# Kernel optimization log

Hardware: AMD Instinct MI355X
Metric: run time of the kernel (lower is better)

## Reference

```python
import jax, jax.numpy as jnp
import numpy as np

D_MODEL = 128
NUM_HEADS = 8
HEAD_DIM = D_MODEL // NUM_HEADS
LN_EPS = 1e-5


def layernorm(x, gamma, beta):
    mu = jnp.mean(x, axis=-1, keepdims=True)
    var = jnp.mean(jnp.square(x - mu), axis=-1, keepdims=True)
    return (x - mu) * jax.lax.rsqrt(var + LN_EPS) * gamma + beta


def setup_inputs() -> dict:
    key = jax.random.key(0)
    ks = jax.random.split(key, 12)
    B, L, d = 16, 1024, D_MODEL
    scale = 1.0 / np.sqrt(d)
    edge_x = jax.random.normal(ks[0], (B, L, d), dtype=jnp.float32)
    # True entries are masked out (masked_fill with -inf)
    edge_mask = jax.random.randint(ks[1], (B, L, L), 0, 2).astype(jnp.bool_)
    in_proj_w = jax.random.normal(ks[2], (d, 3 * d), dtype=jnp.float32) * scale  # fused QKV
    in_proj_b = jnp.zeros((3 * d,), dtype=jnp.float32)
    w1 = jax.random.normal(ks[3], (d, d), dtype=jnp.float32) * scale
    b1 = jnp.zeros((d,), dtype=jnp.float32)
    w2 = jax.random.normal(ks[4], (d, d), dtype=jnp.float32) * scale
    b2 = jnp.zeros((d,), dtype=jnp.float32)
    g1 = jnp.ones((d,), dtype=jnp.float32)
    beta1 = jnp.zeros((d,), dtype=jnp.float32)
    g2 = jnp.ones((d,), dtype=jnp.float32)
    beta2 = jnp.zeros((d,), dtype=jnp.float32)
    return {"edge_x": edge_x, "edge_mask": edge_mask, "in_proj_w": in_proj_w,
            "in_proj_b": in_proj_b, "w1": w1, "b1": b1, "w2": w2, "b2": b2,
            "g1": g1, "beta1": beta1, "g2": g2, "beta2": beta2}


def reference(edge_x, edge_mask, in_proj_w, in_proj_b, w1, b1, w2, b2, g1, beta1, g2, beta2):
    B, L, d = edge_x.shape
    H, hd = NUM_HEADS, HEAD_DIM
    scaling = float(hd) ** -0.5
    # fused QKV projection
    qkv = edge_x @ in_proj_w + in_proj_b              # [B, L, 3d]
    q, k, v = jnp.split(qkv, 3, axis=-1)
    q = q.reshape(B, L, H, hd).transpose(0, 2, 1, 3)  # [B, H, L, hd]
    k = k.reshape(B, L, H, hd).transpose(0, 2, 1, 3)
    v = v.reshape(B, L, H, hd).transpose(0, 2, 1, 3)
    scores = jnp.einsum('bhqd,bhkd->bhqk', q, k) * scaling  # [B, H, L, L]
    scores = jnp.where(edge_mask[:, None, :, :], -jnp.inf, scores)
    attn = jax.nn.softmax(scores, axis=-1)
    ctx = jnp.einsum('bhqk,bhkd->bhqd', attn, v)      # [B, H, L, hd]
    ctx = ctx.transpose(0, 2, 1, 3).reshape(B, L, d)
    # residual + LayerNorm
    x = layernorm(edge_x + ctx, g1, beta1)
    # FFN (relu), residual + LayerNorm (dropout=0 in eval mode)
    ff = jax.nn.relu(x @ w1 + b1) @ w2 + b2
    x = layernorm(x + ff, g2, beta2)
    return x
```

## Files before the change

### kernel.cpp

```cpp
#include <hip/hip_runtime.h>
#include <cstdint>

#define NROWS 16384
#define ARRE ((size_t)NROWS * 128)

typedef short short8 __attribute__((ext_vector_type(8)));
typedef float f32x4  __attribute__((ext_vector_type(4)));
typedef float f32x16 __attribute__((ext_vector_type(16)));

static __device__ __forceinline__ unsigned short f2bf(float f) {
    union { float f; uint32_t u; } v; v.f = f;
    uint32_t r = v.u + 0x7fffu + ((v.u >> 16) & 1u);
    return (unsigned short)(r >> 16);
}

__global__ void k_detect(const uint32_t* __restrict__ m, int* __restrict__ flag) {
    if (threadIdx.x == 0) {
        int f = 0;
        for (int i = 0; i < 256; ++i) f |= (m[i] > 1u) ? 1 : 0;
        *flag = f;
    }
}

__global__ void k_castw(const float* __restrict__ wqkv, const float* __restrict__ w1,
                        const float* __restrict__ w2, unsigned short* __restrict__ wT)
{
    const int e = blockIdx.x * 256 + threadIdx.x;
    if (e < 49152) {
        const int n = e >> 7, k = e & 127;
        wT[e] = f2bf(wqkv[k * 384 + n]);
    } else if (e < 65536) {
        const int i = e - 49152, n = i >> 7, k = i & 127;
        wT[e] = f2bf(w1[k * 128 + n]);
    } else if (e < 81920) {
        const int i = e - 65536, n = i >> 7, k = i & 127;
        wT[e] = f2bf(w2[k * 128 + n]);
    }
}

template<int NF, int MODE>
__global__ __launch_bounds__(256, 2) void k_mm(const float* __restrict__ Xf,
        const unsigned short* __restrict__ Wt, const float* __restrict__ bias,
        unsigned short* __restrict__ out)
{
    __shared__ char smem[16384 + NF * 4096];
    char* const sX = smem;
    char* const sW = smem + 16384;
    const int t = threadIdx.x;
    const int w = t >> 6, l = t & 63;
    const int l4 = l >> 4, l15 = l & 15;
    const int r0 = blockIdx.x * 64;
    const int c0 = blockIdx.y * (NF * 16);

    #pragma unroll
    for (int i = 0; i < 4; ++i) {
        const int c = t + 256 * i;
        const int row = c >> 4, slot = c & 15;
        const float4* src = (const float4*)(Xf + (size_t)(r0 + row) * 128 + slot * 8);
        float4 f0 = src[0], f1 = src[1];
        uint4 v;
        v.x = (uint32_t)f2bf(f0.x) | ((uint32_t)f2bf(f0.y) << 16);
        v.y = (uint32_t)f2bf(f0.z) | ((uint32_t)f2bf(f0.w) << 16);
        v.z = (uint32_t)f2bf(f1.x) | ((uint32_t)f2bf(f1.y) << 16);
        v.w = (uint32_t)f2bf(f1.z) | ((uint32_t)f2bf(f1.w) << 16);
        *(uint4*)(sX + row * 256 + ((slot ^ (row & 15)) << 4)) = v;
    }
    #pragma unroll
    for (int i = 0; i < NF; ++i) {
        const int c = t + 256 * i;
        const int col = c >> 4, slot = c & 15;
        uint4 v = *(const uint4*)(Wt + (size_t)(c0 + col) * 128 + slot * 8);
        *(uint4*)(sW + col * 256 + ((slot ^ (col & 15)) << 4)) = v;
    }
    __syncthreads();

    short8 aF[4];
    #pragma unroll
    for (int kk = 0; kk < 4; ++kk)
        aF[kk] = *(const short8*)(sX + (w * 16 + l15) * 256 + (((kk * 4 + l4) ^ l15) << 4));

    f32x4 acc[NF];
    #pragma unroll
    for (int nf = 0; nf < NF; ++nf) acc[nf] = f32x4{0.f, 0.f, 0.f, 0.f};
    #pragma unroll
    for (int nf = 0; nf < NF; ++nf) {
        #pragma unroll
        for (int kk = 0; kk < 4; ++kk) {
            short8 bF = *(const short8*)(sW + (nf * 16 + l15) * 256 + (((kk * 4 + l4) ^ l15) << 4));
            acc[nf] = __builtin_amdgcn_mfma_f32_16x16x32_bf16(aF[kk], bF, acc[nf], 0, 0, 0);
        }
    }

    const float scl = (MODE == 0 && blockIdx.y == 0) ? 0.25f : 1.0f;
    #pragma unroll
    for (int nf = 0; nf < NF; ++nf) {
        const int col = c0 + nf * 16 + l15;
        const float bv = bias[col];
        #pragma unroll
        for (int reg = 0; reg < 4; ++reg) {
            float v = acc[nf][reg] + bv;
            if (MODE == 1) v = fmaxf(v, 0.f);
            v *= scl;
            const int row = r0 + w * 16 + l4 * 4 + reg;
            size_t o;
            if (MODE == 0) o = (size_t)(col >> 7) * ARRE + (size_t)row * 128 + (col & 127);
            else           o = (size_t)row * 128 + col;
            out[o] = f2bf(v);
        }
    }
}

__global__ __launch_bounds__(256, 2) void k_mm2(const unsigned short* __restrict__ h1,
        const unsigned short* __restrict__ w2t, const float* __restrict__ b2,
        const float* __restrict__ x1, const float* __restrict__ g2,
        const float* __restrict__ be2, float* __restrict__ out)
{
    __shared__ char smem[16384 + 32768];
    char* const sX = smem;
    char* const sW = smem + 16384;
    const int t = threadIdx.x;
    const int w = t >> 6, l = t & 63;
    const int l4 = l >> 4, l15 = l & 15;
    const int r0 = blockIdx.x * 64;

    #pragma unroll
    for (int i = 0; i < 4; ++i) {
        const int c = t + 256 * i;
        const int row = c >> 4, slot = c & 15;
        uint4 v = *(const uint4*)(h1 + (size_t)(r0 + row) * 128 + slot * 8);
        *(uint4*)(sX + row * 256 + ((slot ^ (row & 15)) << 4)) = v;
    }
    #pragma unroll
    for (int i = 0; i < 8; ++i) {
        const int c = t + 256 * i;
        const int col = c >> 4, slot = c & 15;
        uint4 v = *(const uint4*)(w2t + (size_t)col * 128 + slot * 8);
        *(uint4*)(sW + col * 256 + ((slot ^ (col & 15)) << 4)) = v;
    }
    __syncthreads();

    short8 aF[4];
    #pragma unroll
    for (int kk = 0; kk < 4; ++kk)
        aF[kk] = *(const short8*)(sX + (w * 16 + l15) * 256 + (((kk * 4 + l4) ^ l15) << 4));

    f32x4 acc[8];
    #pragma unroll
    for (int nf = 0; nf < 8; ++nf) acc[nf] = f32x4{0.f, 0.f, 0.f, 0.f};
    #pragma unroll
    for (int nf = 0; nf < 8; ++nf) {
        #pragma unroll
        for (int kk = 0; kk < 4; ++kk) {
            short8 bF = *(const short8*)(sW + (nf * 16 + l15) * 256 + (((kk * 4 + l4) ^ l15) << 4));
            acc[nf] = __builtin_amdgcn_mfma_f32_16x16x32_bf16(aF[kk], bF, acc[nf], 0, 0, 0);
        }
    }

    float b2c[8], g2c[8], bec[8];
    #pragma unroll
    for (int nf = 0; nf < 8; ++nf) {
        const int col = nf * 16 + l15;
        b2c[nf] = b2[col]; g2c[nf] = g2[col]; bec[nf] = be2[col];
    }
    float y[8][4];
    #pragma unroll
    for (int nf = 0; nf < 8; ++nf) {
        const int col = nf * 16 + l15;
        #pragma unroll
        for (int reg = 0; reg < 4; ++reg) {
            const int row = r0 + w * 16 + l4 * 4 + reg;
            y[nf][reg] = acc[nf][reg] + b2c[nf] + x1[(size_t)row * 128 + col];
        }
    }
    #pragma unroll
    for (int reg = 0; reg < 4; ++reg) {
        float s = 0.f;
        #pragma unroll
        for (int nf = 0; nf < 8; ++nf) s += y[nf][reg];
        s += __shfl_xor(s, 1); s += __shfl_xor(s, 2);
        s += __shfl_xor(s, 4); s += __shfl_xor(s, 8);
        const float mu = s * (1.f / 128.f);
        float vv = 0.f;
        #pragma unroll
        for (int nf = 0; nf < 8; ++nf) { float d = y[nf][reg] - mu; vv += d * d; }
        vv += __shfl_xor(vv, 1); vv += __shfl_xor(vv, 2);
        vv += __shfl_xor(vv, 4); vv += __shfl_xor(vv, 8);
        const float rs = rsqrtf(vv * (1.f / 128.f) + 1e-5f);
        const int row = r0 + w * 16 + l4 * 4 + reg;
        #pragma unroll
        for (int nf = 0; nf < 8; ++nf) {
            const int col = nf * 16 + l15;
            out[(size_t)row * 128 + col] = (y[nf][reg] - mu) * rs * g2c[nf] + bec[nf];
        }
    }
}

__global__ __launch_bounds__(256, 2) void k_attn(
        const unsigned short* __restrict__ qb,
        const unsigned short* __restrict__ kb,
        const unsigned short* __restrict__ vbp,
        const void* __restrict__ maskp, const int* __restrict__ flag,
        const float* __restrict__ x, const float* __restrict__ g1,
        const float* __restrict__ be1, float* __restrict__ x1)
{
    __shared__ alignas(16) char smem[39072];
    char*          const sK = smem;
    char*          const sV = smem + 8192;
    char*          const sP = smem + 17440;
    unsigned char* const sM = (unsigned char*)(smem + 37920);
    float*         const sS = (float*)(smem + 38048);

    const int t  = threadIdx.x;
    const int w  = t >> 6;
    const int l  = t & 63;
    const int b  = blockIdx.y;
    const int q0 = blockIdx.x * 32;
    const int q   = l & 31;
    const int hi  = l >> 5;
    const int l4  = l >> 4;
    const int l15 = l & 15;
    const int bytemask = *flag;

    short8 qf0, qf1;
    {
        const size_t qrow = (size_t)(b * 1024 + q0 + q) * 128;
        qf0 = *(const short8*)(qb + qrow + (2 * w + 0) * 16 + hi * 8);
        qf1 = *(const short8*)(qb + qrow + (2 * w + 1) * 16 + hi * 8);
    }
    float m0 = -INFINITY, m1 = -INFINITY;
    float ls0 = 0.f, ls1 = 0.f;
    f32x4 a00 = {0,0,0,0}, a01 = {0,0,0,0}, a10 = {0,0,0,0}, a11 = {0,0,0,0};
    const f32x16 z16 = {};
    float* const sS0 = sS + (w * 2 + 0) * 32;
    float* const sS1 = sS + (w * 2 + 1) * 32;
    char*  const sP0 = sP + (w * 2 + 0) * 2560;
    char*  const sP1 = sP + (w * 2 + 1) * 2560;

    const uint8_t* m8  = (const uint8_t*)maskp;
    const int*     m32 = (const int*)maskp;

    uint32_t mks = 0;

    auto head_step = [&](int h, short8 qf, float& m, float& ls,
                         f32x4& ac0, f32x4& ac1, float* sSw, char* Pw) {
        short8 kf = *(const short8*)(sK + q * 256 + ((((h << 1) + hi) ^ (q & 15)) << 4));
        f32x16 sc = __builtin_amdgcn_mfma_f32_32x32x16_bf16(kf, qf, z16, 0, 0, 0);
        float sm = sc[0];
        #pragma unroll
        for (int r = 1; r < 16; ++r) sm = fmaxf(sm, sc[r]);
        sm = fmaxf(sm, __shfl_xor(sm, 32));
        if (__any(sm > m + 8.f)) {
            float nm = fmaxf(m, sm);
            float s  = __expf(m - nm);
            m = nm; ls *= s;
            sSw[q] = s;
            float4 s0v = *(float4*)&sSw[l4 * 4];
            float4 s1v = *(float4*)&sSw[l4 * 4 + 16];
            ac0[0] *= s0v.x; ac0[1] *= s0v.y; ac0[2] *= s0v.z; ac0[3] *= s0v.w;
            ac1[0] *= s1v.x; ac1[1] *= s1v.y; ac1[2] *= s1v.z; ac1[3] *= s1v.w;
        }
        float p[16]; float lsum = 0.f;
        #pragma unroll
        for (int r = 0; r < 16; ++r) {
            const int c = (r & 3) + 8 * (r >> 2);
            float pv = __expf(sc[r] - m);
            pv = ((mks >> c) & 1u) ? pv : 0.f;
            lsum += pv; p[r] = pv;
        }
        ls += lsum;
        #pragma unroll
        for (int g = 0; g < 4; ++g) {
            uint2 pk;
            pk.x = (uint32_t)f2bf(p[4*g+0]) | ((uint32_t)f2bf(p[4*g+1]) << 16);
            pk.y = (uint32_t)f2bf(p[4*g+2]) | ((uint32_t)f2bf(p[4*g+3]) << 16);
            *(uint2*)(Pw + q * 80 + (8 * g + 4 * hi) * 2) = pk;
        }
        short8 pa0 = *(const short8*)(Pw + l15 * 80 + l4 * 16);
        short8 pa1 = *(const short8*)(Pw + (l15 + 16) * 80 + l4 * 16);
        const unsigned short* sVh = (const unsigned short*)(sV + h * 1156);
        short8 vf;
        #pragma unroll
        for (int j = 0; j < 8; ++j)
            vf[j] = (short)sVh[(l4 * 8 + j) * 18 + l15];
        ac0 = __builtin_amdgcn_mfma_f32_16x16x32_bf16(pa0, vf, ac0, 0, 0, 0);
        ac1 = __builtin_amdgcn_mfma_f32_16x16x32_bf16(pa1, vf, ac1, 0, 0, 0);
    };

    for (int kt = 0; kt < 32; ++kt) {
        const int k0 = kt * 32;
        __syncthreads();
        #pragma unroll
        for (int i = 0; i < 2; ++i) {
            const int idx = t + 256 * i;
            const int row = idx >> 4, slot = idx & 15;
            const size_t src = (size_t)(b * 1024 + k0 + row) * 128 + slot * 8;
            uint4 kv = *(const uint4*)(kb + src);
            *(uint4*)(sK + row * 256 + ((slot ^ (row & 15)) << 4)) = kv;
            uint4 vv = *(const uint4*)(vbp + src);
            unsigned short* dh = (unsigned short*)(sV + (slot >> 1) * 1156);
            uint32_t* dst = (uint32_t*)(dh + row * 18 + (slot & 1) * 8);
            dst[0] = vv.x; dst[1] = vv.y; dst[2] = vv.z; dst[3] = vv.w;
        }
        {
            const int mq = t >> 3, g = t & 7;
            if (g < 4) {
                const size_t moff = ((size_t)b << 20) + (size_t)(q0 + mq) * 1024
                                  + (size_t)(k0 + g * 8);
                unsigned int bits = 0;
                if (bytemask) {
                    uint64_t v = *(const uint64_t*)(m8 + moff);
                    #pragma unroll
                    for (int j = 0; j < 8; ++j)
                        bits |= ((((v >> (8 * j)) & 0xffull) == 0ull) ? 1u : 0u) << j;
                } else {
                    const int4* p = (const int4*)(m32 + moff);
                    int4 va = p[0], vc = p[1];
                    bits = (va.x==0?1u:0u) | (va.y==0?2u:0u) | (va.z==0?4u:0u) | (va.w==0?8u:0u)
                         | (vc.x==0?16u:0u) | (vc.y==0?32u:0u) | (vc.z==0?64u:0u) | (vc.w==0?128u:0u);
                }
                sM[mq * 4 + g] = (unsigned char)bits;
            }
        }
        __syncthreads();

        const uint32_t mk = *(const uint32_t*)(sM + q * 4);
        mks = mk >> (4 * hi);

        head_step(2 * w + 0, qf0, m0, ls0, a00, a01, sS0, sP0);
        head_step(2 * w + 1, qf1, m1, ls1, a10, a11, sS1, sP1);
    }

    __syncthreads();
    float* const sC = (float*)smem;
    auto finish = [&](int h, float ls, f32x4 ac0, f32x4 ac1, float* sSw) {
        float lt  = ls + __shfl_xor(ls, 32);
        float inv = 1.f / lt;
        sSw[q] = inv;
        float4 i0 = *(float4*)&sSw[l4 * 4];
        float4 i1 = *(float4*)&sSw[l4 * 4 + 16];
        const int cc = h * 16 + l15;
        sC[(l4 * 4 + 0) * 132 + cc]  = ac0[0] * i0.x;
        sC[(l4 * 4 + 1) * 132 + cc]  = ac0[1] * i0.y;
        sC[(l4 * 4 + 2) * 132 + cc]  = ac0[2] * i0.z;
        sC[(l4 * 4 + 3) * 132 + cc]  = ac0[3] * i0.w;
        sC[(l4 * 4 + 16) * 132 + cc] = ac1[0] * i1.x;
        sC[(l4 * 4 + 17) * 132 + cc] = ac1[1] * i1.y;
        sC[(l4 * 4 + 18) * 132 + cc] = ac1[2] * i1.z;
        sC[(l4 * 4 + 19) * 132 + cc] = ac1[3] * i1.w;
    };
    finish(2 * w + 0, ls0, a00, a01, sS0);
    finish(2 * w + 1, ls1, a10, a11, sS1);
    __syncthreads();

    {
        const int row = w * 8 + (l >> 3);
        const int c0  = (l & 7) * 16;
        const size_t grow = (size_t)(b * 1024 + q0 + row);
        const float4* xp = (const float4*)(x + grow * 128 + c0);
        const float4* cp = (const float4*)(sC + row * 132 + c0);
        float y[16];
        float s = 0.f;
        #pragma unroll
        for (int j = 0; j < 4; ++j) {
            float4 xv = xp[j], cv = cp[j];
            y[4*j+0] = xv.x + cv.x; y[4*j+1] = xv.y + cv.y;
            y[4*j+2] = xv.z + cv.z; y[4*j+3] = xv.w + cv.w;
            s += y[4*j+0] + y[4*j+1] + y[4*j+2] + y[4*j+3];
        }
        s += __shfl_xor(s, 1); s += __shfl_xor(s, 2); s += __shfl_xor(s, 4);
        const float mu = s * (1.f / 128.f);
        float vv = 0.f;
        #pragma unroll
        for (int e = 0; e < 16; ++e) { float d = y[e] - mu; vv += d * d; }
        vv += __shfl_xor(vv, 1); vv += __shfl_xor(vv, 2); vv += __shfl_xor(vv, 4);
        const float rs = rsqrtf(vv * (1.f / 128.f) + 1e-5f);
        #pragma unroll
        for (int j = 0; j < 4; ++j) {
            float4 gv = *(const float4*)(g1 + c0 + 4 * j);
            float4 bv = *(const float4*)(be1 + c0 + 4 * j);
            float4 o;
            o.x = (y[4*j+0] - mu) * rs * gv.x + bv.x;
            o.y = (y[4*j+1] - mu) * rs * gv.y + bv.y;
            o.z = (y[4*j+2] - mu) * rs * gv.z + bv.z;
            o.w = (y[4*j+3] - mu) * rs * gv.w + bv.w;
            *(float4*)(x1 + grow * 128 + c0 + 4 * j) = o;
        }
    }
}

extern "C" void kernel_launch(void* const* d_in, const int* in_sizes, int n_in,
                              void* d_out, int out_size, void* d_ws, size_t ws_size,
                              hipStream_t stream)
{
    const float* x    = (const float*)d_in[0];
    const void*  mask = d_in[1];
    const float* wqkv = (const float*)d_in[2];
    const float* bqkv = (const float*)d_in[3];
    const float* w1   = (const float*)d_in[4];
    const float* b1   = (const float*)d_in[5];
    const float* w2   = (const float*)d_in[6];
    const float* b2   = (const float*)d_in[7];
    const float* g1   = (const float*)d_in[8];
    const float* be1  = (const float*)d_in[9];
    const float* g2   = (const float*)d_in[10];
    const float* be2  = (const float*)d_in[11];
    float* out = (float*)d_out;

    char* base = (char*)d_ws;
    int* flag = (int*)base;
    unsigned short* qb  = (unsigned short*)(base + 256);
    unsigned short* kb  = qb + ARRE;
    unsigned short* vb  = kb + ARRE;
    float* x1           = (float*)(base + 256 + (size_t)12 * 1024 * 1024);
    unsigned short* wT  = (unsigned short*)(base + 256 + (size_t)20 * 1024 * 1024);
    unsigned short* h1b = qb;

    k_detect<<<1, 64, 0, stream>>>((const uint32_t*)mask, flag);
    k_castw<<<320, 256, 0, stream>>>(wqkv, w1, w2, wT);
    k_mm<8, 0><<<dim3(256, 3), 256, 0, stream>>>(x, wT, bqkv, qb);
    k_attn<<<dim3(32, 16), 256, 0, stream>>>(qb, kb, vb, mask, flag, x, g1, be1, x1);
    k_mm<4, 1><<<dim3(256, 2), 256, 0, stream>>>(x1, wT + 49152, b1, h1b);
    k_mm2<<<256, 256, 0, stream>>>(h1b, wT + 65536, b2, x1, g2, be2, out);
}
```

Measured before the change: 211.4 us.

## Use one wave per head in attention, transpose MFMA outputs for vectorized stores

The attention kernel moves from 256 threads handling two heads per wave to 512 threads with one head per wave. This gives more waves to hide latency, at the cost of more registers and LDS pressure per block. The GEMM kernels swap the MFMA operand order so each lane owns a row and four consecutive columns, which allows packed bf16 uint2 stores and float4 bias, residual and LayerNorm loads with cheaper cross-lane reductions. Scalar bf16 rounding is replaced with the hardware v_cvt_pk_bf16_f32 instruction.

```diff
diff --git a/kernel.cpp b/kernel.cpp
--- a/kernel.cpp
+++ b/kernel.cpp
@@ -12,6 +12,12 @@
     union { float f; uint32_t u; } v; v.f = f;
     uint32_t r = v.u + 0x7fffu + ((v.u >> 16) & 1u);
     return (unsigned short)(r >> 16);
+}
+
+static __device__ __forceinline__ uint32_t cvt_pk_bf16(float lo, float hi) {
+    uint32_t r;
+    asm("v_cvt_pk_bf16_f32 %0, %1, %2" : "=v"(r) : "v"(lo), "v"(hi));
+    return r;
 }
 
 __global__ void k_detect(const uint32_t* __restrict__ m, int* __restrict__ flag) {
@@ -59,10 +65,10 @@
         const float4* src = (const float4*)(Xf + (size_t)(r0 + row) * 128 + slot * 8);
         float4 f0 = src[0], f1 = src[1];
         uint4 v;
-        v.x = (uint32_t)f2bf(f0.x) | ((uint32_t)f2bf(f0.y) << 16);
-        v.y = (uint32_t)f2bf(f0.z) | ((uint32_t)f2bf(f0.w) << 16);
-        v.z = (uint32_t)f2bf(f1.x) | ((uint32_t)f2bf(f1.y) << 16);
-        v.w = (uint32_t)f2bf(f1.z) | ((uint32_t)f2bf(f1.w) << 16);
+        v.x = cvt_pk_bf16(f0.x, f0.y);
+        v.y = cvt_pk_bf16(f0.z, f0.w);
+        v.z = cvt_pk_bf16(f1.x, f1.y);
+        v.w = cvt_pk_bf16(f1.z, f1.w);
         *(uint4*)(sX + row * 256 + ((slot ^ (row & 15)) << 4)) = v;
     }
     #pragma unroll
@@ -87,26 +93,30 @@
         #pragma unroll
         for (int kk = 0; kk < 4; ++kk) {
             short8 bF = *(const short8*)(sW + (nf * 16 + l15) * 256 + (((kk * 4 + l4) ^ l15) << 4));
-            acc[nf] = __builtin_amdgcn_mfma_f32_16x16x32_bf16(aF[kk], bF, acc[nf], 0, 0, 0);
+            acc[nf] = __builtin_amdgcn_mfma_f32_16x16x32_bf16(bF, aF[kk], acc[nf], 0, 0, 0);
         }
     }
 
     const float scl = (MODE == 0 && blockIdx.y == 0) ? 0.25f : 1.0f;
+    const int row = r0 + w * 16 + l15;
     #pragma unroll
     for (int nf = 0; nf < NF; ++nf) {
-        const int col = c0 + nf * 16 + l15;
-        const float bv = bias[col];
-        #pragma unroll
-        for (int reg = 0; reg < 4; ++reg) {
-            float v = acc[nf][reg] + bv;
-            if (MODE == 1) v = fmaxf(v, 0.f);
-            v *= scl;
-            const int row = r0 + w * 16 + l4 * 4 + reg;
-            size_t o;
-            if (MODE == 0) o = (size_t)(col >> 7) * ARRE + (size_t)row * 128 + (col & 127);
-            else           o = (size_t)row * 128 + col;
-            out[o] = f2bf(v);
-        }
+        const int cb = nf * 16 + l4 * 4;
+        float4 bv = *(const float4*)(bias + c0 + cb);
+        float v0 = acc[nf][0] + bv.x, v1 = acc[nf][1] + bv.y;
+        float v2 = acc[nf][2] + bv.z, v3 = acc[nf][3] + bv.w;
+        if (MODE == 1) {
+            v0 = fmaxf(v0, 0.f); v1 = fmaxf(v1, 0.f);
+            v2 = fmaxf(v2, 0.f); v3 = fmaxf(v3, 0.f);
+        }
+        v0 *= scl; v1 *= scl; v2 *= scl; v3 *= scl;
+        uint2 pk;
+        pk.x = cvt_pk_bf16(v0, v1);
+        pk.y = cvt_pk_bf16(v2, v3);
+        size_t o;
+        if (MODE == 0) o = (size_t)blockIdx.y * ARRE + (size_t)row * 128 + cb;
+        else           o = (size_t)row * 128 + c0 + cb;
+        *(uint2*)(out + o) = pk;
     }
 }
 
@@ -152,50 +162,49 @@
         #pragma unroll
         for (int kk = 0; kk < 4; ++kk) {
             short8 bF = *(const short8*)(sW + (nf * 16 + l15) * 256 + (((kk * 4 + l4) ^ l15) << 4));
-            acc[nf] = __builtin_amdgcn_mfma_f32_16x16x32_bf16(aF[kk], bF, acc[nf], 0, 0, 0);
-        }
-    }
-
-    float b2c[8], g2c[8], bec[8];
+            acc[nf] = __builtin_amdgcn_mfma_f32_16x16x32_bf16(bF, aF[kk], acc[nf], 0, 0, 0);
+        }
+    }
+
+    const int row = r0 + w * 16 + l15;
+    float y[8][4];
+    float s = 0.f;
     #pragma unroll
     for (int nf = 0; nf < 8; ++nf) {
-        const int col = nf * 16 + l15;
-        b2c[nf] = b2[col]; g2c[nf] = g2[col]; bec[nf] = be2[col];
-    }
-    float y[8][4];
+        const int cb = nf * 16 + l4 * 4;
+        float4 bv = *(const float4*)(b2 + cb);
+        float4 xv = *(const float4*)(x1 + (size_t)row * 128 + cb);
+        y[nf][0] = acc[nf][0] + bv.x + xv.x;
+        y[nf][1] = acc[nf][1] + bv.y + xv.y;
+        y[nf][2] = acc[nf][2] + bv.z + xv.z;
+        y[nf][3] = acc[nf][3] + bv.w + xv.w;
+        s += y[nf][0] + y[nf][1] + y[nf][2] + y[nf][3];
+    }
+    s += __shfl_xor(s, 16); s += __shfl_xor(s, 32);
+    const float mu = s * (1.f / 128.f);
+    float vv = 0.f;
     #pragma unroll
     for (int nf = 0; nf < 8; ++nf) {
-        const int col = nf * 16 + l15;
-        #pragma unroll
-        for (int reg = 0; reg < 4; ++reg) {
-            const int row = r0 + w * 16 + l4 * 4 + reg;
-            y[nf][reg] = acc[nf][reg] + b2c[nf] + x1[(size_t)row * 128 + col];
-        }
-    }
-    #pragma unroll
-    for (int reg = 0; reg < 4; ++reg) {
-        float s = 0.f;
-        #pragma unroll
-        for (int nf = 0; nf < 8; ++nf) s += y[nf][reg];
-        s += __shfl_xor(s, 1); s += __shfl_xor(s, 2);
-        s += __shfl_xor(s, 4); s += __shfl_xor(s, 8);
-        const float mu = s * (1.f / 128.f);
-        float vv = 0.f;
-        #pragma unroll
-        for (int nf = 0; nf < 8; ++nf) { float d = y[nf][reg] - mu; vv += d * d; }
-        vv += __shfl_xor(vv, 1); vv += __shfl_xor(vv, 2);
-        vv += __shfl_xor(vv, 4); vv += __shfl_xor(vv, 8);
-        const float rs = rsqrtf(vv * (1.f / 128.f) + 1e-5f);
-        const int row = r0 + w * 16 + l4 * 4 + reg;
-        #pragma unroll
-        for (int nf = 0; nf < 8; ++nf) {
-            const int col = nf * 16 + l15;
-            out[(size_t)row * 128 + col] = (y[nf][reg] - mu) * rs * g2c[nf] + bec[nf];
-        }
-    }
-}
-
-__global__ __launch_bounds__(256, 2) void k_attn(
+        #pragma unroll
+        for (int reg = 0; reg < 4; ++reg) { float d = y[nf][reg] - mu; vv += d * d; }
+    }
+    vv += __shfl_xor(vv, 16); vv += __shfl_xor(vv, 32);
+    const float rs = rsqrtf(vv * (1.f / 128.f) + 1e-5f);
+    #pragma unroll
+    for (int nf = 0; nf < 8; ++nf) {
+        const int cb = nf * 16 + l4 * 4;
+        float4 gv = *(const float4*)(g2 + cb);
+        float4 ev = *(const float4*)(be2 + cb);
+        float4 o;
+        o.x = (y[nf][0] - mu) * rs * gv.x + ev.x;
+        o.y = (y[nf][1] - mu) * rs * gv.y + ev.y;
+        o.z = (y[nf][2] - mu) * rs * gv.z + ev.z;
+        o.w = (y[nf][3] - mu) * rs * gv.w + ev.w;
+        *(float4*)(out + (size_t)row * 128 + cb) = o;
+    }
+}
+
+__global__ __launch_bounds__(512, 2) void k_attn(
         const unsigned short* __restrict__ qb,
         const unsigned short* __restrict__ kb,
         const unsigned short* __restrict__ vbp,
@@ -221,29 +230,57 @@
     const int l15 = l & 15;
     const int bytemask = *flag;
 
-    short8 qf0, qf1;
+    short8 qf;
     {
         const size_t qrow = (size_t)(b * 1024 + q0 + q) * 128;
-        qf0 = *(const short8*)(qb + qrow + (2 * w + 0) * 16 + hi * 8);
-        qf1 = *(const short8*)(qb + qrow + (2 * w + 1) * 16 + hi * 8);
-    }
-    float m0 = -INFINITY, m1 = -INFINITY;
-    float ls0 = 0.f, ls1 = 0.f;
-    f32x4 a00 = {0,0,0,0}, a01 = {0,0,0,0}, a10 = {0,0,0,0}, a11 = {0,0,0,0};
+        qf = *(const short8*)(qb + qrow + w * 16 + hi * 8);
+    }
+    float m = -INFINITY, ls = 0.f;
+    f32x4 ac0 = {0,0,0,0}, ac1 = {0,0,0,0};
     const f32x16 z16 = {};
-    float* const sS0 = sS + (w * 2 + 0) * 32;
-    float* const sS1 = sS + (w * 2 + 1) * 32;
-    char*  const sP0 = sP + (w * 2 + 0) * 2560;
-    char*  const sP1 = sP + (w * 2 + 1) * 2560;
+    float* const sSw = sS + w * 32;
+    char*  const Pw  = sP + w * 2560;
 
     const uint8_t* m8  = (const uint8_t*)maskp;
     const int*     m32 = (const int*)maskp;
 
-    uint32_t mks = 0;
-
-    auto head_step = [&](int h, short8 qf, float& m, float& ls,
-                         f32x4& ac0, f32x4& ac1, float* sSw, char* Pw) {
-        short8 kf = *(const short8*)(sK + q * 256 + ((((h << 1) + hi) ^ (q & 15)) << 4));
+    for (int kt = 0; kt < 32; ++kt) {
+        const int k0 = kt * 32;
+        __syncthreads();
+        {
+            const int row = t >> 4, slot = t & 15;
+            const size_t src = (size_t)(b * 1024 + k0 + row) * 128 + slot * 8;
+            uint4 kv = *(const uint4*)(kb + src);
+            *(uint4*)(sK + row * 256 + ((slot ^ (row & 15)) << 4)) = kv;
+            uint4 vv = *(const uint4*)(vbp + src);
+            unsigned short* dh = (unsigned short*)(sV + (slot >> 1) * 1156);
+            uint32_t* dst = (uint32_t*)(dh + row * 18 + (slot & 1) * 8);
+            dst[0] = vv.x; dst[1] = vv.y; dst[2] = vv.z; dst[3] = vv.w;
+        }
+        if (t < 128) {
+            const int mq = t >> 2, g = t & 3;
+            const size_t moff = ((size_t)b << 20) + (size_t)(q0 + mq) * 1024
+                              + (size_t)(k0 + g * 8);
+            unsigned int bits = 0;
+            if (bytemask) {
+                uint64_t v = *(const uint64_t*)(m8 + moff);
+                #pragma unroll
+                for (int j = 0; j < 8; ++j)
+                    bits |= ((((v >> (8 * j)) & 0xffull) == 0ull) ? 1u : 0u) << j;
+            } else {
+                const int4* p = (const int4*)(m32 + moff);
+                int4 va = p[0], vc = p[1];
+                bits = (va.x==0?1u:0u) | (va.y==0?2u:0u) | (va.z==0?4u:0u) | (va.w==0?8u:0u)
+                     | (vc.x==0?16u:0u) | (vc.y==0?32u:0u) | (vc.z==0?64u:0u) | (vc.w==0?128u:0u);
+            }
+            sM[mq * 4 + g] = (unsigned char)bits;
+        }
+        __syncthreads();
+
+        const uint32_t mk = *(const uint32_t*)(sM + q * 4);
+        const uint32_t mks = mk >> (4 * hi);
+
+        short8 kf = *(const short8*)(sK + q * 256 + ((((w << 1) + hi) ^ (q & 15)) << 4));
         f32x16 sc = __builtin_amdgcn_mfma_f32_32x32x16_bf16(kf, qf, z16, 0, 0, 0);
         float sm = sc[0];
         #pragma unroll
@@ -271,74 +308,30 @@
         #pragma unroll
         for (int g = 0; g < 4; ++g) {
             uint2 pk;
-            pk.x = (uint32_t)f2bf(p[4*g+0]) | ((uint32_t)f2bf(p[4*g+1]) << 16);
-            pk.y = (uint32_t)f2bf(p[4*g+2]) | ((uint32_t)f2bf(p[4*g+3]) << 16);
+            pk.x = cvt_pk_bf16(p[4*g+0], p[4*g+1]);
+            pk.y = cvt_pk_bf16(p[4*g+2], p[4*g+3]);
             *(uint2*)(Pw + q * 80 + (8 * g + 4 * hi) * 2) = pk;
         }
         short8 pa0 = *(const short8*)(Pw + l15 * 80 + l4 * 16);
         short8 pa1 = *(const short8*)(Pw + (l15 + 16) * 80 + l4 * 16);
-        const unsigned short* sVh = (const unsigned short*)(sV + h * 1156);
+        const unsigned short* sVh = (const unsigned short*)(sV + w * 1156);
         short8 vf;
         #pragma unroll
         for (int j = 0; j < 8; ++j)
             vf[j] = (short)sVh[(l4 * 8 + j) * 18 + l15];
         ac0 = __builtin_amdgcn_mfma_f32_16x16x32_bf16(pa0, vf, ac0, 0, 0, 0);
         ac1 = __builtin_amdgcn_mfma_f32_16x16x32_bf16(pa1, vf, ac1, 0, 0, 0);
-    };
-
-    for (int kt = 0; kt < 32; ++kt) {
-        const int k0 = kt * 32;
-        __syncthreads();
-        #pragma unroll
-        for (int i = 0; i < 2; ++i) {
-            const int idx = t + 256 * i;
-            const int row = idx >> 4, slot = idx & 15;
-            const size_t src = (size_t)(b * 1024 + k0 + row) * 128 + slot * 8;
-            uint4 kv = *(const uint4*)(kb + src);
-            *(uint4*)(sK + row * 256 + ((slot ^ (row & 15)) << 4)) = kv;
-            uint4 vv = *(const uint4*)(vbp + src);
-            unsigned short* dh = (unsigned short*)(sV + (slot >> 1) * 1156);
-            uint32_t* dst = (uint32_t*)(dh + row * 18 + (slot & 1) * 8);
-            dst[0] = vv.x; dst[1] = vv.y; dst[2] = vv.z; dst[3] = vv.w;
-        }
-        {
-            const int mq = t >> 3, g = t & 7;
-            if (g < 4) {
-                const size_t moff = ((size_t)b << 20) + (size_t)(q0 + mq) * 1024
-                                  + (size_t)(k0 + g * 8);
-                unsigned int bits = 0;
-                if (bytemask) {
-                    uint64_t v = *(const uint64_t*)(m8 + moff);
-                    #pragma unroll
-                    for (int j = 0; j < 8; ++j)
-                        bits |= ((((v >> (8 * j)) & 0xffull) == 0ull) ? 1u : 0u) << j;
-                } else {
-                    const int4* p = (const int4*)(m32 + moff);
-                    int4 va = p[0], vc = p[1];
-                    bits = (va.x==0?1u:0u) | (va.y==0?2u:0u) | (va.z==0?4u:0u) | (va.w==0?8u:0u)
-                         | (vc.x==0?16u:0u) | (vc.y==0?32u:0u) | (vc.z==0?64u:0u) | (vc.w==0?128u:0u);
-                }
-                sM[mq * 4 + g] = (unsigned char)bits;
-            }
-        }
-        __syncthreads();
-
-        const uint32_t mk = *(const uint32_t*)(sM + q * 4);
-        mks = mk >> (4 * hi);
-
-        head_step(2 * w + 0, qf0, m0, ls0, a00, a01, sS0, sP0);
-        head_step(2 * w + 1, qf1, m1, ls1, a10, a11, sS1, sP1);
     }
 
     __syncthreads();
     float* const sC = (float*)smem;
-    auto finish = [&](int h, float ls, f32x4 ac0, f32x4 ac1, float* sSw) {
+    {
         float lt  = ls + __shfl_xor(ls, 32);
         float inv = 1.f / lt;
         sSw[q] = inv;
         float4 i0 = *(float4*)&sSw[l4 * 4];
         float4 i1 = *(float4*)&sSw[l4 * 4 + 16];
-        const int cc = h * 16 + l15;
+        const int cc = w * 16 + l15;
         sC[(l4 * 4 + 0) * 132 + cc]  = ac0[0] * i0.x;
         sC[(l4 * 4 + 1) * 132 + cc]  = ac0[1] * i0.y;
         sC[(l4 * 4 + 2) * 132 + cc]  = ac0[2] * i0.z;
@@ -347,35 +340,35 @@
         sC[(l4 * 4 + 17) * 132 + cc] = ac1[1] * i1.y;
         sC[(l4 * 4 + 18) * 132 + cc] = ac1[2] * i1.z;
         sC[(l4 * 4 + 19) * 132 + cc] = ac1[3] * i1.w;
-    };
-    finish(2 * w + 0, ls0, a00, a01, sS0);
-    finish(2 * w + 1, ls1, a10, a11, sS1);
+    }
     __syncthreads();
 
     {
-        const int row = w * 8 + (l >> 3);
-        const int c0  = (l & 7) * 16;
+        const int row = t >> 4;
+        const int c0  = (t & 15) * 8;
         const size_t grow = (size_t)(b * 1024 + q0 + row);
         const float4* xp = (const float4*)(x + grow * 128 + c0);
         const float4* cp = (const float4*)(sC + row * 132 + c0);
-        float y[16];
+        float y[8];
         float s = 0.f;
         #pragma unroll
-        for (int j = 0; j < 4; ++j) {
+        for (int j = 0; j < 2; ++j) {
             float4 xv = xp[j], cv = cp[j];
             y[4*j+0] = xv.x + cv.x; y[4*j+1] = xv.y + cv.y;
             y[4*j+2] = xv.z + cv.z; y[4*j+3] = xv.w + cv.w;
             s += y[4*j+0] + y[4*j+1] + y[4*j+2] + y[4*j+3];
         }
-        s += __shfl_xor(s, 1); s += __shfl_xor(s, 2); s += __shfl_xor(s, 4);
+        s += __shfl_xor(s, 1); s += __shfl_xor(s, 2);
+        s += __shfl_xor(s, 4); s += __shfl_xor(s, 8);
         const float mu = s * (1.f / 128.f);
         float vv = 0.f;
         #pragma unroll
-        for (int e = 0; e < 16; ++e) { float d = y[e] - mu; vv += d * d; }
-        vv += __shfl_xor(vv, 1); vv += __shfl_xor(vv, 2); vv += __shfl_xor(vv, 4);
+        for (int e = 0; e < 8; ++e) { float d = y[e] - mu; vv += d * d; }
+        vv += __shfl_xor(vv, 1); vv += __shfl_xor(vv, 2);
+        vv += __shfl_xor(vv, 4); vv += __shfl_xor(vv, 8);
         const float rs = rsqrtf(vv * (1.f / 128.f) + 1e-5f);
         #pragma unroll
-        for (int j = 0; j < 4; ++j) {
+        for (int j = 0; j < 2; ++j) {
             float4 gv = *(const float4*)(g1 + c0 + 4 * j);
             float4 bv = *(const float4*)(be1 + c0 + 4 * j);
             float4 o;
@@ -418,7 +411,7 @@
     k_detect<<<1, 64, 0, stream>>>((const uint32_t*)mask, flag);
     k_castw<<<320, 256, 0, stream>>>(wqkv, w1, w2, wT);
     k_mm<8, 0><<<dim3(256, 3), 256, 0, stream>>>(x, wT, bqkv, qb);
-    k_attn<<<dim3(32, 16), 256, 0, stream>>>(qb, kb, vb, mask, flag, x, g1, be1, x1);
+    k_attn<<<dim3(32, 16), 512, 0, stream>>>(qb, kb, vb, mask, flag, x, g1, be1, x1);
     k_mm<4, 1><<<dim3(256, 2), 256, 0, stream>>>(x1, wT + 49152, b1, h1b);
     k_mm2<<<256, 256, 0, stream>>>(h1b, wT + 65536, b2, x1, g2, be2, out);
 }
```

Measured after the change: 196.9 us. 1.07x faster.
